# Performance work log

Hardware: AMD Instinct MI355X
Metric: run time of the kernel (lower is better)

Reference implementation:

```python
import jax, jax.numpy as jnp
import numpy as np

D_IN = 1024
D_OUT = 1024
NUM_HEADS = 16
HEAD_DIM = D_OUT // NUM_HEADS
WINDOW = 256


def setup_inputs() -> dict:
    key = jax.random.key(0)
    ks = jax.random.split(key, 6)
    s = 0.02
    x = jax.random.normal(ks[0], (2, 2048, D_IN), dtype=jnp.float32)
    Wq = jax.random.normal(ks[1], (D_IN, D_OUT), dtype=jnp.float32) * s
    Wk = jax.random.normal(ks[2], (D_IN, D_OUT), dtype=jnp.float32) * s
    Wv = jax.random.normal(ks[3], (D_IN, D_OUT), dtype=jnp.float32) * s
    Wo = jax.random.normal(ks[4], (D_OUT, D_OUT), dtype=jnp.float32) * s
    bo = jnp.zeros((D_OUT,), dtype=jnp.float32)
    return {"x": x, "Wq": Wq, "Wk": Wk, "Wv": Wv, "Wo": Wo, "bo": bo}


def reference(x, Wq, Wk, Wv, Wo, bo):
    b, s, _ = x.shape
    # project and split heads: [b, h, s, hd]
    def heads(t):
        return t.reshape(b, s, NUM_HEADS, HEAD_DIM).transpose(0, 2, 1, 3)
    q = heads(x @ Wq)
    k = heads(x @ Wk)
    v = heads(x @ Wv)
    scores = jnp.einsum('bhqd,bhkd->bhqk', q, k) / jnp.sqrt(jnp.float32(HEAD_DIM))
    # symmetric sliding-window band: |i - j| <= WINDOW
    i = jnp.arange(s)
    band = jnp.abs(i[:, None] - i[None, :]) <= WINDOW  # [s, s]
    scores = jnp.where(band[None, None], scores, -jnp.inf)
    probs = jax.nn.softmax(scores, axis=-1)  # dropout=0.0 -> identity
    ctx = jnp.einsum('bhqk,bhkd->bhqd', probs, v)
    ctx = ctx.transpose(0, 2, 1, 3).reshape(b, s, D_OUT)
    return ctx @ Wo + bo
```

## Files before the change

kernel.cpp:

```cpp
#include <hip/hip_runtime.h>
#include <hip/hip_bf16.h>

typedef __bf16 bf16_t;
typedef __bf16 bf16x8 __attribute__((ext_vector_type(8)));
typedef __bf16 bf16x4 __attribute__((ext_vector_type(4)));
typedef float  f32x4  __attribute__((ext_vector_type(4)));

#define SEQ    2048
#define BATCH  2
#define NHEAD  16
#define HDIM   64
#define DMODEL 1024
#define WIN    256

__device__ __forceinline__ void async_load16(const void* g, void* l) {
    __builtin_amdgcn_global_load_lds(
        (const __attribute__((address_space(1))) char*)(uintptr_t)g,
        (__attribute__((address_space(3))) char*)(uintptr_t)l, 16, 0, 0);
}

__global__ void cast_x_kernel(const float* __restrict__ x, bf16_t* __restrict__ xb, int n4) {
    int i = blockIdx.x * blockDim.x + threadIdx.x;
    if (i >= n4) return;
    float4 v = ((const float4*)x)[i];
    bf16x4 o;
    o[0] = (bf16_t)v.x; o[1] = (bf16_t)v.y; o[2] = (bf16_t)v.z; o[3] = (bf16_t)v.w;
    ((bf16x4*)xb)[i] = o;
}

__global__ void transpose_w_kernel(const float* __restrict__ Wq, const float* __restrict__ Wk,
                                   const float* __restrict__ Wv, const float* __restrict__ Wo,
                                   bf16_t* __restrict__ Wt) {
    __shared__ float tile[32][33];
    const float* W = (blockIdx.z == 0) ? Wq : (blockIdx.z == 1) ? Wk : (blockIdx.z == 2) ? Wv : Wo;
    bf16_t* out = Wt + (size_t)blockIdx.z * DMODEL * DMODEL;
    int k0 = blockIdx.y * 32, n0 = blockIdx.x * 32;
    int tx = threadIdx.x, ty = threadIdx.y;
#pragma unroll
    for (int i = 0; i < 4; i++)
        tile[ty + i * 8][tx] = W[(size_t)(k0 + ty + i * 8) * DMODEL + n0 + tx];
    __syncthreads();
#pragma unroll
    for (int i = 0; i < 4; i++)
        out[(size_t)(n0 + ty + i * 8) * DMODEL + k0 + tx] = (bf16_t)tile[tx][ty + i * 8];
}

__global__ __launch_bounds__(256) void vtrans_kernel(const bf16_t* __restrict__ Vb,
                                                     bf16_t* __restrict__ Vt) {
    __shared__ bf16_t tile[64][65];
    const int bh = blockIdx.y, s0 = blockIdx.x * 64;
    const int tx = threadIdx.x, ty = threadIdx.y;
    const bf16_t* src = Vb + ((size_t)bh * SEQ + s0) * HDIM;
    bf16_t* dst = Vt + (size_t)bh * HDIM * SEQ + s0;
#pragma unroll
    for (int i = 0; i < 16; i++) {
        int row = i * 4 + ty;
        tile[row][tx] = src[(size_t)row * HDIM + tx];
    }
    __syncthreads();
#pragma unroll
    for (int i = 0; i < 16; i++) {
        int d = i * 4 + ty;
        dst[(size_t)d * SEQ + tx] = tile[tx][d];
    }
}

template <int EPI>
__global__ __launch_bounds__(256) void gemm_bt_kernel(
    const bf16_t* __restrict__ A, const bf16_t* __restrict__ Bt,
    bf16_t* __restrict__ Qb, bf16_t* __restrict__ Kb, bf16_t* __restrict__ Vb,
    float* __restrict__ Out, const float* __restrict__ bo, int K, int nPer) {
    __shared__ __attribute__((aligned(16))) bf16_t As[128 * 64];
    __shared__ __attribute__((aligned(16))) bf16_t Bs[128 * 64];
    const int tid = threadIdx.x;
    const int wave = tid >> 6, lane = tid & 63, quad = lane >> 4, l15 = lane & 15;
    const int wm = wave >> 1, wn = wave & 1;
    const int id = blockIdx.x, xcd = id & 7, t = id >> 3;
    const int m0 = (t / nPer) * 128, n0 = (xcd * nPer + t % nPer) * 128;

    f32x4 acc[4][4] = {};

    for (int kt = 0; kt < K; kt += 64) {
#pragma unroll
        for (int i = 0; i < 4; i++) {
            int v = tid + i * 256;
            int row = v >> 3, c = (v & 7) ^ (row & 7);
            async_load16(A + (size_t)(m0 + row) * K + kt + c * 8, (char*)As + (size_t)v * 16);
            async_load16(Bt + (size_t)(n0 + row) * K + kt + c * 8, (char*)Bs + (size_t)v * 16);
        }
        __syncthreads();
#pragma unroll
        for (int kk = 0; kk < 64; kk += 32) {
            bf16x8 am[4], bn[4];
#pragma unroll
            for (int i = 0; i < 4; i++) {
                int row = wm * 64 + i * 16 + l15;
                int ch = ((kk >> 3) + quad) ^ (row & 7);
                am[i] = *(const bf16x8*)&As[row * 64 + ch * 8];
            }
#pragma unroll
            for (int j = 0; j < 4; j++) {
                int row = wn * 64 + j * 16 + l15;
                int ch = ((kk >> 3) + quad) ^ (row & 7);
                bn[j] = *(const bf16x8*)&Bs[row * 64 + ch * 8];
            }
#pragma unroll
            for (int i = 0; i < 4; i++)
#pragma unroll
                for (int j = 0; j < 4; j++)
                    acc[i][j] = __builtin_amdgcn_mfma_f32_16x16x32_bf16(am[i], bn[j], acc[i][j], 0, 0, 0);
        }
        __syncthreads();
    }

#pragma unroll
    for (int i = 0; i < 4; i++)
#pragma unroll
        for (int j = 0; j < 4; j++)
#pragma unroll
            for (int r = 0; r < 4; r++) {
                int mg = m0 + wm * 64 + i * 16 + quad * 4 + r;
                int ng = n0 + wn * 64 + j * 16 + l15;
                float v = acc[i][j][r];
                if (EPI == 0) {
                    int sel = ng >> 10, nl = ng & 1023, h = nl >> 6, d = nl & 63;
                    int b = mg >> 11, s = mg & 2047;
                    size_t idx = ((size_t)((b * NHEAD + h) * SEQ) + s) * HDIM + d;
                    if (sel == 0)      Qb[idx] = (bf16_t)(v * 0.18033688011112042f);
                    else if (sel == 1) Kb[idx] = (bf16_t)v;
                    else               Vb[idx] = (bf16_t)v;
                } else {
                    Out[(size_t)mg * DMODEL + ng] = v + bo[ng];
                }
            }
}

__global__ __launch_bounds__(512) void attn_kernel(
    const bf16_t* __restrict__ Qb, const bf16_t* __restrict__ Kb,
    const bf16_t* __restrict__ Vt, bf16_t* __restrict__ ctx) {
    __shared__ __attribute__((aligned(16))) bf16_t Ks[2][64 * 64];
    __shared__ __attribute__((aligned(16))) bf16_t Vs[2][64 * 64];
    __shared__ __attribute__((aligned(16))) bf16_t Plds[8][16][72];
    const int tid = threadIdx.x;
    const int wave = tid >> 6, lane = tid & 63, quad = lane >> 4, l15 = lane & 15;

    const int id = blockIdx.x;
    const int task = (id & 7) * 64 + (id >> 3);
    const int b = task >> 8, h = (task >> 4) & 15, Q0 = (task & 15) << 7;
    const int qbase = Q0 + wave * 16;
    const int wqt = (Q0 >> 6) + (wave >> 2);

    const bf16_t* Qp = Qb + (size_t)(b * NHEAD + h) * SEQ * HDIM;
    const bf16_t* Kp = Kb + (size_t)(b * NHEAD + h) * SEQ * HDIM;
    const bf16_t* Vp = Vt + (size_t)(b * NHEAD + h) * HDIM * SEQ;

    bf16x8 qa0 = *(const bf16x8*)(Qp + (size_t)(qbase + l15) * HDIM + quad * 8);
    bf16x8 qa1 = *(const bf16x8*)(Qp + (size_t)(qbase + l15) * HDIM + 32 + quad * 8);

    bf16x8 ones;
#pragma unroll
    for (int j = 0; j < 8; j++) ones[j] = (bf16_t)1.0f;

    f32x4 O[4] = {};
    f32x4 lacc = {};

    const int base_t = Q0 >> 6;
    const int bt0 = (base_t - 4 > 0) ? base_t - 4 : 0;
    const int bt1 = (base_t + 5 < SEQ / 64 - 1) ? base_t + 5 : SEQ / 64 - 1;

    auto stage = [&](int kt, int buf) {
        const int k0 = kt * 64;
        int v = tid;
        int row = v >> 3, c = (v & 7) ^ (row & 7);
        async_load16(Kp + (size_t)(k0 + row) * HDIM + c * 8, (char*)&Ks[buf][0] + (size_t)v * 16);
        async_load16(Vp + (size_t)row * SEQ + k0 + c * 8, (char*)&Vs[buf][0] + (size_t)v * 16);
    };

    stage(bt0, 0);
    int cb = 0;
    for (int kt = bt0; kt <= bt1; kt++) {
        __syncthreads();
        if (kt < bt1) stage(kt + 1, cb ^ 1);
        const int dt = kt - wqt;
        if (dt >= -4 && dt <= 4) {
            const int k0 = kt * 64;
            f32x4 st[4];
#pragma unroll
            for (int c = 0; c < 4; c++) {
                int row = c * 16 + l15;
                bf16x8 kb0 = *(const bf16x8*)&Ks[cb][row * 64 + (quad ^ (row & 7)) * 8];
                bf16x8 kb1 = *(const bf16x8*)&Ks[cb][row * 64 + ((quad + 4) ^ (row & 7)) * 8];
                f32x4 a = {};
                a = __builtin_amdgcn_mfma_f32_16x16x32_bf16(kb0, qa0, a, 0, 0, 0);
                a = __builtin_amdgcn_mfma_f32_16x16x32_bf16(kb1, qa1, a, 0, 0, 0);
                st[c] = a;
            }
            const bool edge = (dt == -4 || dt == 4);
            const int q = qbase + l15;
#pragma unroll
            for (int c = 0; c < 4; c++) {
                bf16x4 pk;
#pragma unroll
                for (int r = 0; r < 4; r++) {
                    float sv = st[c][r];
                    if (edge) {
                        int k = k0 + c * 16 + quad * 4 + r;
                        int dd = q - k; dd = (dd < 0) ? -dd : dd;
                        if (dd > WIN) sv = -1e30f;
                    }
                    pk[r] = (bf16_t)exp2f(sv);
                }
                *(bf16x4*)&Plds[wave][l15][c * 16 + quad * 4] = pk;
            }
            bf16x8 pa0 = *(const bf16x8*)&Plds[wave][l15][quad * 8];
            bf16x8 pa1 = *(const bf16x8*)&Plds[wave][l15][32 + quad * 8];
            lacc = __builtin_amdgcn_mfma_f32_16x16x32_bf16(pa0, ones, lacc, 0, 0, 0);
            lacc = __builtin_amdgcn_mfma_f32_16x16x32_bf16(pa1, ones, lacc, 0, 0, 0);
#pragma unroll
            for (int d = 0; d < 4; d++) {
                int row = d * 16 + l15;
                bf16x8 vb0 = *(const bf16x8*)&Vs[cb][row * 64 + (quad ^ (row & 7)) * 8];
                bf16x8 vb1 = *(const bf16x8*)&Vs[cb][row * 64 + ((quad + 4) ^ (row & 7)) * 8];
                O[d] = __builtin_amdgcn_mfma_f32_16x16x32_bf16(pa0, vb0, O[d], 0, 0, 0);
                O[d] = __builtin_amdgcn_mfma_f32_16x16x32_bf16(pa1, vb1, O[d], 0, 0, 0);
            }
        }
        cb ^= 1;
    }

#pragma unroll
    for (int r = 0; r < 4; r++) {
        float inv = 1.0f / lacc[r];
        int i = qbase + quad * 4 + r;
#pragma unroll
        for (int d = 0; d < 4; d++) {
            float v = O[d][r] * inv;
            ctx[((size_t)(b * SEQ + i)) * DMODEL + h * HDIM + d * 16 + l15] = (bf16_t)v;
        }
    }
}

extern "C" void kernel_launch(void* const* d_in, const int* in_sizes, int n_in,
                              void* d_out, int out_size, void* d_ws, size_t ws_size,
                              hipStream_t stream) {
    const float* x  = (const float*)d_in[0];
    const float* Wq = (const float*)d_in[1];
    const float* Wk = (const float*)d_in[2];
    const float* Wv = (const float*)d_in[3];
    const float* Wo = (const float*)d_in[4];
    const float* bo = (const float*)d_in[5];
    float* out = (float*)d_out;

    const size_t MTOK = (size_t)BATCH * SEQ;
    bf16_t* xb  = (bf16_t*)d_ws;
    bf16_t* Wt  = xb + MTOK * DMODEL;
    bf16_t* Qb  = Wt + (size_t)4 * DMODEL * DMODEL;
    bf16_t* Kb  = Qb + MTOK * DMODEL;
    bf16_t* Vt  = Kb + MTOK * DMODEL;
    bf16_t* ctx = Vt + MTOK * DMODEL;
    bf16_t* Vb  = ctx;

    cast_x_kernel<<<dim3((MTOK * DMODEL / 4 + 255) / 256), dim3(256), 0, stream>>>(
        x, xb, (int)(MTOK * DMODEL / 4));
    transpose_w_kernel<<<dim3(32, 32, 4), dim3(32, 8), 0, stream>>>(Wq, Wk, Wv, Wo, Wt);
    gemm_bt_kernel<0><<<dim3(768), dim3(256), 0, stream>>>(
        xb, Wt, Qb, Kb, Vb, nullptr, nullptr, DMODEL, 3);
    vtrans_kernel<<<dim3(32, 32), dim3(64, 4), 0, stream>>>(Vb, Vt);
    attn_kernel<<<dim3(512), dim3(512), 0, stream>>>(Qb, Kb, Vt, ctx);
    gemm_bt_kernel<1><<<dim3(256), dim3(256), 0, stream>>>(
        ctx, Wt + (size_t)3 * DMODEL * DMODEL, nullptr, nullptr, nullptr, out, bo, DMODEL, 1);
}
```

Before: 175.0 us.

## Fuse prep kernels and rewrite GEMMs with double-buffered pipelined loads

Merges the x cast and weight transpose into one prep kernel that uses 64x64 tiles with vectorized loads and stores. Replaces the QKV projection GEMM with a 256x256-tile, 512-thread kernel that double-buffers LDS, interleaves async global loads between MFMA phases, and raises wave priority during MFMA. The output GEMM gets simple double buffering. This aims to hide global load latency behind MFMA work and cut launch count, at the cost of more LDS per block and fewer blocks for the QKV GEMM.

Measured after the change: 167.6 us. 1.04x faster.

```diff
diff --git a/kernel.cpp b/kernel.cpp
--- a/kernel.cpp
+++ b/kernel.cpp
@@ -19,30 +19,254 @@
         (__attribute__((address_space(3))) char*)(uintptr_t)l, 16, 0, 0);
 }
 
-__global__ void cast_x_kernel(const float* __restrict__ x, bf16_t* __restrict__ xb, int n4) {
-    int i = blockIdx.x * blockDim.x + threadIdx.x;
-    if (i >= n4) return;
-    float4 v = ((const float4*)x)[i];
-    bf16x4 o;
-    o[0] = (bf16_t)v.x; o[1] = (bf16_t)v.y; o[2] = (bf16_t)v.z; o[3] = (bf16_t)v.w;
-    ((bf16x4*)xb)[i] = o;
-}
-
-__global__ void transpose_w_kernel(const float* __restrict__ Wq, const float* __restrict__ Wk,
-                                   const float* __restrict__ Wv, const float* __restrict__ Wo,
-                                   bf16_t* __restrict__ Wt) {
-    __shared__ float tile[32][33];
-    const float* W = (blockIdx.z == 0) ? Wq : (blockIdx.z == 1) ? Wk : (blockIdx.z == 2) ? Wv : Wo;
-    bf16_t* out = Wt + (size_t)blockIdx.z * DMODEL * DMODEL;
-    int k0 = blockIdx.y * 32, n0 = blockIdx.x * 32;
-    int tx = threadIdx.x, ty = threadIdx.y;
+__global__ __launch_bounds__(256) void prep_kernel(
+    const float* __restrict__ x, const float* __restrict__ Wq,
+    const float* __restrict__ Wk, const float* __restrict__ Wv,
+    const float* __restrict__ Wo, bf16_t* __restrict__ xb,
+    bf16_t* __restrict__ Wt) {
+    const int bid = blockIdx.x, tid = threadIdx.x;
+    if (bid < 1024) {
+        __shared__ float t64[64][65];
+        const int mat = bid >> 8, tile = bid & 255;
+        const int k0 = (tile >> 4) * 64, n0 = (tile & 15) * 64;
+        const float* W = (mat == 0) ? Wq : (mat == 1) ? Wk : (mat == 2) ? Wv : Wo;
+        bf16_t* out = Wt + (size_t)mat * DMODEL * DMODEL;
+        const int r = tid >> 4, c4 = tid & 15;
+#pragma unroll
+        for (int i = 0; i < 4; i++) {
+            int krow = i * 16 + r;
+            float4 v = *(const float4*)&W[(size_t)(k0 + krow) * DMODEL + n0 + c4 * 4];
+            t64[krow][c4 * 4 + 0] = v.x; t64[krow][c4 * 4 + 1] = v.y;
+            t64[krow][c4 * 4 + 2] = v.z; t64[krow][c4 * 4 + 3] = v.w;
+        }
+        __syncthreads();
+#pragma unroll
+        for (int j = 0; j < 4; j++) {
+            int nrow = j * 16 + r;
+            bf16x4 o;
+#pragma unroll
+            for (int q = 0; q < 4; q++) o[q] = (bf16_t)t64[c4 * 4 + q][nrow];
+            *(bf16x4*)&out[(size_t)(n0 + nrow) * DMODEL + k0 + c4 * 4] = o;
+        }
+    } else {
+        const int cb = bid - 1024;
+#pragma unroll
+        for (int it = 0; it < 4; it++) {
+            int i = (cb * 4 + it) * 256 + tid;
+            float4 v = ((const float4*)x)[i];
+            bf16x4 o;
+            o[0] = (bf16_t)v.x; o[1] = (bf16_t)v.y; o[2] = (bf16_t)v.z; o[3] = (bf16_t)v.w;
+            ((bf16x4*)xb)[i] = o;
+        }
+    }
+}
+
+__global__ __launch_bounds__(512, 2) void gemm_qkv_kernel(
+    const bf16_t* __restrict__ A, const bf16_t* __restrict__ Bt,
+    bf16_t* __restrict__ Qb, bf16_t* __restrict__ Kb, bf16_t* __restrict__ Vb) {
+    __shared__ __attribute__((aligned(16))) bf16_t smem[2][2][256 * 64];
+    const int tid = threadIdx.x;
+    const int wave = tid >> 6, lane = tid & 63, quad = lane >> 4, l15 = lane & 15;
+    const int wm = wave >> 2, wn = wave & 3;
+    const int id = blockIdx.x, xcd = id & 7, tt = id >> 3;
+    const int gidx = xcd * 24 + tt;
+    const int m0 = (gidx & 15) * 256, n0 = (gidx >> 4) * 256;
+
+    const int cth = (tid & 7) ^ ((tid >> 3) & 7);
+    const int rA = tid >> 3;
+
+    auto stageG = [&](int tile, int gr, int buf) {
+        const int row = (gr & 3) * 64 + rA;
+        const bf16_t* src = (gr < 4)
+            ? A  + (size_t)(m0 + row) * 1024 + tile * 64 + cth * 8
+            : Bt + (size_t)(n0 + row) * 1024 + tile * 64 + cth * 8;
+        async_load16(src, (char*)&smem[buf][gr >> 2][0] + (size_t)((gr & 3) * 512 + tid) * 16);
+    };
+
+    const int swz  = l15 & 7;
+    const int chk0 = (quad ^ swz) * 8;
+    const int chk1 = ((4 + quad) ^ swz) * 8;
+    const int rowA = wm * 128 + l15;
+    const int rowB = wn * 64 + l15;
+
+    f32x4 acc[8][4] = {};
+
+    stageG(0, 4, 0); stageG(0, 5, 0); stageG(0, 6, 0); stageG(0, 7, 0);
+    stageG(0, 0, 0); stageG(0, 2, 0); stageG(0, 1, 0); stageG(0, 3, 0);
+    asm volatile("s_waitcnt vmcnt(2)" ::: "memory");
+    __builtin_amdgcn_s_barrier();
+    __builtin_amdgcn_sched_barrier(0);
+
+    int cur = 0;
+#pragma unroll 1
+    for (int t = 0; t < 16; ++t) {
+        const bf16_t* as = &smem[cur][0][0];
+        const bf16_t* bs = &smem[cur][1][0];
+        bf16x8 am0[4], am1[4], ba0[2], ba1[2], bb0[2], bb1[2];
+#pragma unroll
+        for (int i = 0; i < 4; i++) {
+            am0[i] = *(const bf16x8*)&as[(rowA + i * 16) * 64 + chk0];
+            am1[i] = *(const bf16x8*)&as[(rowA + i * 16) * 64 + chk1];
+        }
+#pragma unroll
+        for (int j = 0; j < 2; j++) {
+            ba0[j] = *(const bf16x8*)&bs[(rowB + j * 16) * 64 + chk0];
+            ba1[j] = *(const bf16x8*)&bs[(rowB + j * 16) * 64 + chk1];
+        }
+        if (t + 1 < 16) { stageG(t + 1, 4, cur ^ 1); stageG(t + 1, 5, cur ^ 1); }
+        __builtin_amdgcn_s_barrier();
+        __builtin_amdgcn_sched_barrier(0);
+        __builtin_amdgcn_s_setprio(1);
+#pragma unroll
+        for (int i = 0; i < 4; i++)
+#pragma unroll
+            for (int j = 0; j < 2; j++) {
+                acc[i][j] = __builtin_amdgcn_mfma_f32_16x16x32_bf16(am0[i], ba0[j], acc[i][j], 0, 0, 0);
+                acc[i][j] = __builtin_amdgcn_mfma_f32_16x16x32_bf16(am1[i], ba1[j], acc[i][j], 0, 0, 0);
+            }
+        __builtin_amdgcn_s_setprio(0);
+        __builtin_amdgcn_s_barrier();
+        __builtin_amdgcn_sched_barrier(0);
+#pragma unroll
+        for (int j = 0; j < 2; j++) {
+            bb0[j] = *(const bf16x8*)&bs[(rowB + (j + 2) * 16) * 64 + chk0];
+            bb1[j] = *(const bf16x8*)&bs[(rowB + (j + 2) * 16) * 64 + chk1];
+        }
+        if (t + 1 < 16) { stageG(t + 1, 6, cur ^ 1); stageG(t + 1, 7, cur ^ 1); }
+        __builtin_amdgcn_s_barrier();
+        __builtin_amdgcn_sched_barrier(0);
+        __builtin_amdgcn_s_setprio(1);
+#pragma unroll
+        for (int i = 0; i < 4; i++)
+#pragma unroll
+            for (int j = 0; j < 2; j++) {
+                acc[i][j + 2] = __builtin_amdgcn_mfma_f32_16x16x32_bf16(am0[i], bb0[j], acc[i][j + 2], 0, 0, 0);
+                acc[i][j + 2] = __builtin_amdgcn_mfma_f32_16x16x32_bf16(am1[i], bb1[j], acc[i][j + 2], 0, 0, 0);
+            }
+        __builtin_amdgcn_s_setprio(0);
+        if (t + 1 < 16) asm volatile("s_waitcnt vmcnt(4)" ::: "memory");
+        else            asm volatile("s_waitcnt vmcnt(0)" ::: "memory");
+        __builtin_amdgcn_s_barrier();
+        __builtin_amdgcn_sched_barrier(0);
+#pragma unroll
+        for (int i = 0; i < 4; i++) {
+            am0[i] = *(const bf16x8*)&as[(rowA + (i + 4) * 16) * 64 + chk0];
+            am1[i] = *(const bf16x8*)&as[(rowA + (i + 4) * 16) * 64 + chk1];
+        }
+        if (t + 1 < 16) { stageG(t + 1, 0, cur ^ 1); stageG(t + 1, 2, cur ^ 1); }
+        __builtin_amdgcn_s_barrier();
+        __builtin_amdgcn_sched_barrier(0);
+        __builtin_amdgcn_s_setprio(1);
+#pragma unroll
+        for (int i = 0; i < 4; i++)
+#pragma unroll
+            for (int j = 0; j < 2; j++) {
+                acc[i + 4][j + 2] = __builtin_amdgcn_mfma_f32_16x16x32_bf16(am0[i], bb0[j], acc[i + 4][j + 2], 0, 0, 0);
+                acc[i + 4][j + 2] = __builtin_amdgcn_mfma_f32_16x16x32_bf16(am1[i], bb1[j], acc[i + 4][j + 2], 0, 0, 0);
+            }
+        __builtin_amdgcn_s_setprio(0);
+        __builtin_amdgcn_s_barrier();
+        __builtin_amdgcn_sched_barrier(0);
+        if (t + 1 < 16) { stageG(t + 1, 1, cur ^ 1); stageG(t + 1, 3, cur ^ 1); }
+        __builtin_amdgcn_s_setprio(1);
+#pragma unroll
+        for (int i = 0; i < 4; i++)
+#pragma unroll
+            for (int j = 0; j < 2; j++) {
+                acc[i + 4][j] = __builtin_amdgcn_mfma_f32_16x16x32_bf16(am0[i], ba0[j], acc[i + 4][j], 0, 0, 0);
+                acc[i + 4][j] = __builtin_amdgcn_mfma_f32_16x16x32_bf16(am1[i], ba1[j], acc[i + 4][j], 0, 0, 0);
+            }
+        __builtin_amdgcn_s_setprio(0);
+        if (t + 1 < 16) {
+            asm volatile("s_waitcnt vmcnt(2)" ::: "memory");
+            __builtin_amdgcn_s_barrier();
+            __builtin_amdgcn_sched_barrier(0);
+        }
+        cur ^= 1;
+    }
+
+#pragma unroll
+    for (int i = 0; i < 8; i++)
+#pragma unroll
+        for (int j = 0; j < 4; j++)
+#pragma unroll
+            for (int r = 0; r < 4; r++) {
+                int mg = m0 + wm * 128 + i * 16 + quad * 4 + r;
+                int ng = n0 + wn * 64 + j * 16 + l15;
+                float v = acc[i][j][r];
+                int sel = ng >> 10, nl = ng & 1023, h = nl >> 6, d = nl & 63;
+                int b = mg >> 11, s = mg & 2047;
+                size_t idx = ((size_t)((b * NHEAD + h) * SEQ) + s) * HDIM + d;
+                if (sel == 0)      Qb[idx] = (bf16_t)(v * 0.18033688011112042f);
+                else if (sel == 1) Kb[idx] = (bf16_t)v;
+                else               Vb[idx] = (bf16_t)v;
+            }
+}
+
+__global__ __launch_bounds__(256) void gemm_out_kernel(
+    const bf16_t* __restrict__ A, const bf16_t* __restrict__ Bt,
+    float* __restrict__ Out, const float* __restrict__ bo) {
+    __shared__ __attribute__((aligned(16))) bf16_t As[2][128 * 64];
+    __shared__ __attribute__((aligned(16))) bf16_t Bs[2][128 * 64];
+    const int tid = threadIdx.x;
+    const int wave = tid >> 6, lane = tid & 63, quad = lane >> 4, l15 = lane & 15;
+    const int wm = wave >> 1, wn = wave & 1;
+    const int id = blockIdx.x, xcd = id & 7, t = id >> 3;
+    const int m0 = t * 128, n0 = xcd * 128;
+
+    auto stage = [&](int kt, int buf) {
+#pragma unroll
+        for (int i = 0; i < 4; i++) {
+            int v = tid + i * 256;
+            int row = v >> 3, c = (v & 7) ^ (row & 7);
+            async_load16(A + (size_t)(m0 + row) * 1024 + kt * 64 + c * 8,
+                         (char*)&As[buf][0] + (size_t)v * 16);
+            async_load16(Bt + (size_t)(n0 + row) * 1024 + kt * 64 + c * 8,
+                         (char*)&Bs[buf][0] + (size_t)v * 16);
+        }
+    };
+
+    f32x4 acc[4][4] = {};
+    stage(0, 0);
+    __syncthreads();
+    int cur = 0;
+    for (int kt = 0; kt < 16; ++kt) {
+        if (kt + 1 < 16) stage(kt + 1, cur ^ 1);
+#pragma unroll
+        for (int kk = 0; kk < 64; kk += 32) {
+            bf16x8 am[4], bn[4];
+#pragma unroll
+            for (int i = 0; i < 4; i++) {
+                int row = wm * 64 + i * 16 + l15;
+                int ch = ((kk >> 3) + quad) ^ (row & 7);
+                am[i] = *(const bf16x8*)&As[cur][row * 64 + ch * 8];
+            }
+#pragma unroll
+            for (int j = 0; j < 4; j++) {
+                int row = wn * 64 + j * 16 + l15;
+                int ch = ((kk >> 3) + quad) ^ (row & 7);
+                bn[j] = *(const bf16x8*)&Bs[cur][row * 64 + ch * 8];
+            }
+#pragma unroll
+            for (int i = 0; i < 4; i++)
+#pragma unroll
+                for (int j = 0; j < 4; j++)
+                    acc[i][j] = __builtin_amdgcn_mfma_f32_16x16x32_bf16(am[i], bn[j], acc[i][j], 0, 0, 0);
+        }
+        __syncthreads();
+        cur ^= 1;
+    }
+
 #pragma unroll
     for (int i = 0; i < 4; i++)
-        tile[ty + i * 8][tx] = W[(size_t)(k0 + ty + i * 8) * DMODEL + n0 + tx];
-    __syncthreads();
-#pragma unroll
-    for (int i = 0; i < 4; i++)
-        out[(size_t)(n0 + ty + i * 8) * DMODEL + k0 + tx] = (bf16_t)tile[tx][ty + i * 8];
+#pragma unroll
+        for (int j = 0; j < 4; j++)
+#pragma unroll
+            for (int r = 0; r < 4; r++) {
+                int mg = m0 + wm * 64 + i * 16 + quad * 4 + r;
+                int ng = n0 + wn * 64 + j * 16 + l15;
+                Out[(size_t)mg * DMODEL + ng] = acc[i][j][r] + bo[ng];
+            }
 }
 
 __global__ __launch_bounds__(256) void vtrans_kernel(const bf16_t* __restrict__ Vb,
@@ -63,76 +287,6 @@
         int d = i * 4 + ty;
         dst[(size_t)d * SEQ + tx] = tile[tx][d];
     }
-}
-
-template <int EPI>
-__global__ __launch_bounds__(256) void gemm_bt_kernel(
-    const bf16_t* __restrict__ A, const bf16_t* __restrict__ Bt,
-    bf16_t* __restrict__ Qb, bf16_t* __restrict__ Kb, bf16_t* __restrict__ Vb,
-    float* __restrict__ Out, const float* __restrict__ bo, int K, int nPer) {
-    __shared__ __attribute__((aligned(16))) bf16_t As[128 * 64];
-    __shared__ __attribute__((aligned(16))) bf16_t Bs[128 * 64];
-    const int tid = threadIdx.x;
-    const int wave = tid >> 6, lane = tid & 63, quad = lane >> 4, l15 = lane & 15;
-    const int wm = wave >> 1, wn = wave & 1;
-    const int id = blockIdx.x, xcd = id & 7, t = id >> 3;
-    const int m0 = (t / nPer) * 128, n0 = (xcd * nPer + t % nPer) * 128;
-
-    f32x4 acc[4][4] = {};
-
-    for (int kt = 0; kt < K; kt += 64) {
-#pragma unroll
-        for (int i = 0; i < 4; i++) {
-            int v = tid + i * 256;
-            int row = v >> 3, c = (v & 7) ^ (row & 7);
-            async_load16(A + (size_t)(m0 + row) * K + kt + c * 8, (char*)As + (size_t)v * 16);
-            async_load16(Bt + (size_t)(n0 + row) * K + kt + c * 8, (char*)Bs + (size_t)v * 16);
-        }
-        __syncthreads();
-#pragma unroll
-        for (int kk = 0; kk < 64; kk += 32) {
-            bf16x8 am[4], bn[4];
-#pragma unroll
-            for (int i = 0; i < 4; i++) {
-                int row = wm * 64 + i * 16 + l15;
-                int ch = ((kk >> 3) + quad) ^ (row & 7);
-                am[i] = *(const bf16x8*)&As[row * 64 + ch * 8];
-            }
-#pragma unroll
-            for (int j = 0; j < 4; j++) {
-                int row = wn * 64 + j * 16 + l15;
-                int ch = ((kk >> 3) + quad) ^ (row & 7);
-                bn[j] = *(const bf16x8*)&Bs[row * 64 + ch * 8];
-            }
-#pragma unroll
-            for (int i = 0; i < 4; i++)
-#pragma unroll
-                for (int j = 0; j < 4; j++)
-                    acc[i][j] = __builtin_amdgcn_mfma_f32_16x16x32_bf16(am[i], bn[j], acc[i][j], 0, 0, 0);
-        }
-        __syncthreads();
-    }
-
-#pragma unroll
-    for (int i = 0; i < 4; i++)
-#pragma unroll
-        for (int j = 0; j < 4; j++)
-#pragma unroll
-            for (int r = 0; r < 4; r++) {
-                int mg = m0 + wm * 64 + i * 16 + quad * 4 + r;
-                int ng = n0 + wn * 64 + j * 16 + l15;
-                float v = acc[i][j][r];
-                if (EPI == 0) {
-                    int sel = ng >> 10, nl = ng & 1023, h = nl >> 6, d = nl & 63;
-                    int b = mg >> 11, s = mg & 2047;
-                    size_t idx = ((size_t)((b * NHEAD + h) * SEQ) + s) * HDIM + d;
-                    if (sel == 0)      Qb[idx] = (bf16_t)(v * 0.18033688011112042f);
-                    else if (sel == 1) Kb[idx] = (bf16_t)v;
-                    else               Vb[idx] = (bf16_t)v;
-                } else {
-                    Out[(size_t)mg * DMODEL + ng] = v + bo[ng];
-                }
-            }
 }
 
 __global__ __launch_bounds__(512) void attn_kernel(
@@ -260,13 +414,10 @@
     bf16_t* ctx = Vt + MTOK * DMODEL;
     bf16_t* Vb  = ctx;
 
-    cast_x_kernel<<<dim3((MTOK * DMODEL / 4 + 255) / 256), dim3(256), 0, stream>>>(
-        x, xb, (int)(MTOK * DMODEL / 4));
-    transpose_w_kernel<<<dim3(32, 32, 4), dim3(32, 8), 0, stream>>>(Wq, Wk, Wv, Wo, Wt);
-    gemm_bt_kernel<0><<<dim3(768), dim3(256), 0, stream>>>(
-        xb, Wt, Qb, Kb, Vb, nullptr, nullptr, DMODEL, 3);
+    prep_kernel<<<dim3(2048), dim3(256), 0, stream>>>(x, Wq, Wk, Wv, Wo, xb, Wt);
+    gemm_qkv_kernel<<<dim3(192), dim3(512), 0, stream>>>(xb, Wt, Qb, Kb, Vb);
     vtrans_kernel<<<dim3(32, 32), dim3(64, 4), 0, stream>>>(Vb, Vt);
     attn_kernel<<<dim3(512), dim3(512), 0, stream>>>(Qb, Kb, Vt, ctx);
-    gemm_bt_kernel<1><<<dim3(256), dim3(256), 0, stream>>>(
-        ctx, Wt + (size_t)3 * DMODEL * DMODEL, nullptr, nullptr, nullptr, out, bo, DMODEL, 1);
-}
+    gemm_out_kernel<<<dim3(256), dim3(256), 0, stream>>>(
+        ctx, Wt + (size_t)3 * DMODEL * DMODEL, out, bo);
+}
```
